# Kernel optimization log

Measured on AMD Instinct MI355X. Metric: run time of the kernel, lower is better.

Reference implementation:

```python
import jax, jax.numpy as jnp
import numpy as np

N_NODES = 20000
N_EDGES = 160000
IN_DIM = 64
HID = 256
EDGE_DIM = 64
SF_DIM = 1  # node_counts_dim = max_cycle - MIN_CYCLE + 1 with MIN_CYCLE==max_cycle (source bug)
N_LAYERS = 3
NUM_GRAPHS = 128
MSG_IN = 2 * HID + 2 * SF_DIM + EDGE_DIM  # 578
UPD_IN = 2 * HID


def setup_inputs() -> dict:
    key = jax.random.key(0)
    ks = jax.random.split(key, 16)
    s = 0.05
    return {
        "x": jax.random.normal(ks[0], (N_NODES, IN_DIM), jnp.float32),
        "node_sf": jax.random.uniform(ks[1], (N_NODES, SF_DIM), jnp.float32),
        "edge_feature": jax.random.normal(ks[2], (N_EDGES, EDGE_DIM), jnp.float32),
        "edge_weight": jax.random.uniform(ks[3], (N_EDGES,), jnp.float32),
        "edge_list": jax.random.randint(ks[4], (N_EDGES, 2), 0, N_NODES, jnp.int32),
        "node2graph": jnp.sort(jax.random.randint(ks[5], (N_NODES,), 0, NUM_GRAPHS, jnp.int32)),
        "Wlin": jax.random.normal(ks[6], (IN_DIM, HID), jnp.float32) * s,
        "blin": jnp.zeros((HID,), jnp.float32),
        "msg_W1": jax.random.normal(ks[7], (N_LAYERS, MSG_IN, HID), jnp.float32) * s,
        "msg_b1": jnp.zeros((N_LAYERS, HID), jnp.float32),
        "msg_W2": jax.random.normal(ks[8], (N_LAYERS, HID, HID), jnp.float32) * s,
        "msg_b2": jnp.zeros((N_LAYERS, HID), jnp.float32),
        "upd_W1": jax.random.normal(ks[9], (N_LAYERS, UPD_IN, HID), jnp.float32) * s,
        "upd_b1": jnp.zeros((N_LAYERS, HID), jnp.float32),
        "upd_W2": jax.random.normal(ks[10], (N_LAYERS, HID, HID), jnp.float32) * s,
        "upd_b2": jnp.zeros((N_LAYERS, HID), jnp.float32),
    }


def reference(x, node_sf, edge_feature, edge_weight, edge_list, node2graph,
              Wlin, blin, msg_W1, msg_b1, msg_W2, msg_b2,
              upd_W1, upd_b1, upd_W2, upd_b2):
    node_in = edge_list[:, 0]
    node_out = edge_list[:, 1]
    h = x @ Wlin + blin  # [N, HID]
    for l in range(N_LAYERS):
        # message: gather endpoint features + structural counts + edge features, 2-layer MLP
        m = jnp.concatenate(
            [h[node_in], h[node_out], node_sf[node_in], node_sf[node_out], edge_feature], axis=-1)
        m = jax.nn.relu(m @ msg_W1[l] + msg_b1[l]) @ msg_W2[l] + msg_b2[l]  # [E, HID]
        # aggregate: weighted scatter-add to destination nodes
        upd = jax.ops.segment_sum(m * edge_weight[:, None], node_out, num_segments=N_NODES)
        # combine: concat + 2-layer MLP, then outer activation
        c = jnp.concatenate([h, upd], axis=-1)
        c = jax.nn.relu(c @ upd_W1[l] + upd_b1[l]) @ upd_W2[l] + upd_b2[l]
        h = jax.nn.relu(c)
    # readout: global add pool per graph
    graph_feature = jax.ops.segment_sum(h, node2graph, num_segments=NUM_GRAPHS)
    return graph_feature
```

## Files before the change

### kernel.cpp

```cpp
#include <hip/hip_runtime.h>
#include <hip/hip_bf16.h>

#define N_NODES   20000
#define N_EDGES   160000
#define IN_DIM    64
#define HID       256
#define EDGE_DIM  64
#define NUM_GRAPHS 128
#define N_LAYERS  3

typedef __attribute__((ext_vector_type(8))) short s16x8;
typedef __attribute__((ext_vector_type(4))) float f32x4;

static __device__ __forceinline__ unsigned short f2bu(float f) {
    union { __hip_bfloat16 h; unsigned short u; } cv;
    cv.h = __float2bfloat16(f);
    return cv.u;
}
static __device__ __forceinline__ s16x8 pack8(const float4 a, const float4 b) {
    s16x8 p;
    p[0] = (short)f2bu(a.x); p[1] = (short)f2bu(a.y);
    p[2] = (short)f2bu(a.z); p[3] = (short)f2bu(a.w);
    p[4] = (short)f2bu(b.x); p[5] = (short)f2bu(b.y);
    p[6] = (short)f2bu(b.z); p[7] = (short)f2bu(b.w);
    return p;
}

#define TILE_SH 8192

__global__ __launch_bounds__(256) void k_deg(const int* __restrict__ el,
                                             int* __restrict__ deg) {
    const int e = blockIdx.x * 256 + threadIdx.x;
    if (e < N_EDGES) atomicAdd(&deg[el[2 * e + 1]], 1);
}

__global__ __launch_bounds__(256) void k_scan(const int* __restrict__ deg,
                                              int* __restrict__ off,
                                              int* __restrict__ cursor) {
    __shared__ int ts[256];
    const int t = threadIdx.x;
    const int base = t * 79;
    const int end  = (base + 79 < N_NODES) ? base + 79 : N_NODES;
    int s = 0;
    for (int i = base; i < end; ++i) s += deg[i];
    ts[t] = s;
    __syncthreads();
    for (int d = 1; d < 256; d <<= 1) {
        const int u = (t >= d) ? ts[t - d] : 0;
        __syncthreads();
        ts[t] += u;
        __syncthreads();
    }
    int run = (t == 0) ? 0 : ts[t - 1];
    for (int i = base; i < end; ++i) {
        off[i] = run; cursor[i] = run; run += deg[i];
    }
}

__global__ __launch_bounds__(256) void k_scat(const int* __restrict__ el,
                                              int* __restrict__ cursor,
                                              int* __restrict__ eidx) {
    const int e = blockIdx.x * 256 + threadIdx.x;
    if (e < N_EDGES) {
        const int d = el[2 * e + 1];
        const int p = atomicAdd(&cursor[d], 1);
        eidx[p] = e;
    }
}

__global__ __launch_bounds__(256) void k_prep(const float* __restrict__ mW1,
                                              const float* __restrict__ mW2,
                                              const float* __restrict__ uW1,
                                              const float* __restrict__ uW2,
                                              unsigned short* __restrict__ msgW1T,
                                              unsigned short* __restrict__ msgW2T,
                                              unsigned short* __restrict__ updW1T,
                                              unsigned short* __restrict__ updW2T) {
    const int b = blockIdx.x;
    const int l = b / 50, t = b % 50;
    const float* W; unsigned short* dst; int rowbase;
    if (t < 18) {
        W = mW1 + (size_t)l * 578 * 256;
        dst = msgW1T + ((size_t)l * 18 + t) * TILE_SH;
        rowbase = (t < 16) ? t * 32 : 514 + (t - 16) * 32;
    } else if (t < 26) {
        const int tt = t - 18;
        W = mW2 + (size_t)l * 65536;
        dst = msgW2T + ((size_t)l * 8 + tt) * TILE_SH;
        rowbase = tt * 32;
    } else if (t < 42) {
        const int tt = t - 26;
        W = uW1 + (size_t)l * 131072;
        dst = updW1T + ((size_t)l * 16 + tt) * TILE_SH;
        rowbase = tt * 32;
    } else {
        const int tt = t - 42;
        W = uW2 + (size_t)l * 65536;
        dst = updW2T + ((size_t)l * 8 + tt) * TILE_SH;
        rowbase = tt * 32;
    }
    const int c = threadIdx.x;
    unsigned short buf[32];
    #pragma unroll
    for (int kk = 0; kk < 32; ++kk)
        buf[kk] = f2bu(W[(size_t)(rowbase + kk) * 256 + c]);
    #pragma unroll
    for (int j = 0; j < 4; ++j)
        *(s16x8*)&dst[(size_t)c * 32 + j * 8] = *(const s16x8*)&buf[j * 8];
}

__global__ __launch_bounds__(256) void k_lin(const float* __restrict__ x,
                                             const float* __restrict__ W,
                                             const float* __restrict__ b,
                                             float* __restrict__ h) {
    __shared__ float Xs[16][68];
    const int tid = threadIdx.x;
    const int n0  = blockIdx.x * 16;
    {
        const int row = tid >> 4, q = tid & 15;
        const float4 v = *(const float4*)&x[(size_t)(n0 + row) * IN_DIM + q * 4];
        Xs[row][q * 4 + 0] = v.x; Xs[row][q * 4 + 1] = v.y;
        Xs[row][q * 4 + 2] = v.z; Xs[row][q * 4 + 3] = v.w;
    }
    __syncthreads();
    const int col = tid;
    float acc[16];
    #pragma unroll
    for (int r = 0; r < 16; ++r) acc[r] = 0.f;
    for (int k = 0; k < IN_DIM; ++k) {
        const float w = W[(size_t)k * HID + col];
        #pragma unroll
        for (int r = 0; r < 16; ++r) acc[r] += Xs[r][k] * w;
    }
    const float bb = b[col];
    #pragma unroll
    for (int r = 0; r < 16; ++r) h[(size_t)(n0 + r) * HID + col] = acc[r] + bb;
}

__global__ __launch_bounds__(256, 3) void k_msg(const float* __restrict__ h,
                                                const float* __restrict__ sf,
                                                const float* __restrict__ ef,
                                                const float* __restrict__ ew,
                                                const int*   __restrict__ el,
                                                const int*   __restrict__ eidx,
                                                const unsigned short* __restrict__ W1T,
                                                const float* __restrict__ W1f,
                                                const float* __restrict__ b1,
                                                const unsigned short* __restrict__ W2T,
                                                const float* __restrict__ b2,
                                                float* __restrict__ upd) {
    __shared__ unsigned short As[2][64 * 40];
    __shared__ __align__(16) unsigned short Ts[64 * 264];
    __shared__ int   Se[64], Sni[64], Sno[64];
    __shared__ float Sew[64], Ssa[64], Ssb[64];

    const int tid = threadIdx.x;
    const int e0  = blockIdx.x * 64;
    if (tid < 64) {
        const int e = eidx[e0 + tid];
        const int a = el[2 * e], bn = el[2 * e + 1];
        Se[tid] = e; Sni[tid] = a; Sno[tid] = bn;
        Sew[tid] = ew[e]; Ssa[tid] = sf[a]; Ssb[tid] = sf[bn];
    }
    __syncthreads();

    const int lane = tid & 63, wv = tid >> 6;
    const int lr = lane & 15, lq = lane >> 4;
    const int arow = tid & 63, aq = tid >> 6;
    const int ni = Sni[arow], no = Sno[arow], myE = Se[arow];

    const unsigned short* bp1 = W1T + ((size_t)(wv * 64 + lr)) * 32 + lq * 8;
    const unsigned short* bp2 = W2T + ((size_t)(wv * 64 + lr)) * 32 + lq * 8;

    f32x4 acc[4][4];
    #pragma unroll
    for (int i = 0; i < 4; ++i)
        #pragma unroll
        for (int j = 0; j < 4; ++j) acc[i][j] = (f32x4)(0.0f);

    {
        const float* asrc = h + (size_t)ni * HID + aq * 8;
        const float4 a0 = *(const float4*)(asrc);
        const float4 a1 = *(const float4*)(asrc + 4);
        *(s16x8*)&As[0][arow * 40 + aq * 8] = pack8(a0, a1);
    }
    s16x8 bfr[4], nbr[4];
    #pragma unroll
    for (int nf = 0; nf < 4; ++nf)
        bfr[nf] = *(const s16x8*)(bp1 + nf * 512);
    __syncthreads();

    for (int s = 0; s < 18; ++s) {
        s16x8 af[4];
        #pragma unroll
        for (int mf = 0; mf < 4; ++mf)
            af[mf] = *(const s16x8*)&As[s & 1][(mf * 16 + lr) * 40 + lq * 8];
        const bool hasNext = (s + 1 < 18);
        float4 nA0, nA1;
        if (hasNext) {
            const int sn = s + 1;
            const float* asrc;
            if (sn < 8)       asrc = h  + (size_t)ni * HID + sn * 32;
            else if (sn < 16) asrc = h  + (size_t)no * HID + (sn - 8) * 32;
            else              asrc = ef + (size_t)myE * EDGE_DIM + (sn - 16) * 32;
            nA0 = *(const float4*)(asrc + aq * 8);
            nA1 = *(const float4*)(asrc + aq * 8 + 4);
            #pragma unroll
            for (int nf = 0; nf < 4; ++nf)
                nbr[nf] = *(const s16x8*)(bp1 + (size_t)sn * TILE_SH + nf * 512);
        }
        #pragma unroll
        for (int mf = 0; mf < 4; ++mf)
            #pragma unroll
            for (int nf = 0; nf < 4; ++nf)
                acc[mf][nf] = __builtin_amdgcn_mfma_f32_16x16x32_bf16(
                    af[mf], bfr[nf], acc[mf][nf], 0, 0, 0);
        if (hasNext) {
            *(s16x8*)&As[(s + 1) & 1][arow * 40 + aq * 8] = pack8(nA0, nA1);
            #pragma unroll
            for (int nf = 0; nf < 4; ++nf) bfr[nf] = nbr[nf];
            __syncthreads();
        }
    }

    #pragma unroll
    for (int nf = 0; nf < 4; ++nf) {
        const int col = wv * 64 + nf * 16 + lr;
        const float w512 = W1f[(size_t)512 * HID + col];
        const float w513 = W1f[(size_t)513 * HID + col];
        const float bb   = b1[col];
        #pragma unroll
        for (int mf = 0; mf < 4; ++mf)
            #pragma unroll
            for (int r = 0; r < 4; ++r) {
                const int row = mf * 16 + lq * 4 + r;
                float v = acc[mf][nf][r] + Ssa[row] * w512 + Ssb[row] * w513 + bb;
                Ts[row * 264 + col] = f2bu(fmaxf(v, 0.f));
            }
    }
    __syncthreads();

    f32x4 acc2[4][4];
    #pragma unroll
    for (int i = 0; i < 4; ++i)
        #pragma unroll
        for (int j = 0; j < 4; ++j) acc2[i][j] = (f32x4)(0.0f);

    s16x8 b2f[4], n2b[4];
    #pragma unroll
    for (int nf = 0; nf < 4; ++nf)
        b2f[nf] = *(const s16x8*)(bp2 + nf * 512);

    for (int s = 0; s < 8; ++s) {
        s16x8 af[4];
        #pragma unroll
        for (int mf = 0; mf < 4; ++mf)
            af[mf] = *(const s16x8*)&Ts[(mf * 16 + lr) * 264 + s * 32 + lq * 8];
        if (s + 1 < 8) {
            #pragma unroll
            for (int nf = 0; nf < 4; ++nf)
                n2b[nf] = *(const s16x8*)(bp2 + (size_t)(s + 1) * TILE_SH + nf * 512);
        }
        #pragma unroll
        for (int mf = 0; mf < 4; ++mf)
            #pragma unroll
            for (int nf = 0; nf < 4; ++nf)
                acc2[mf][nf] = __builtin_amdgcn_mfma_f32_16x16x32_bf16(
                    af[mf], b2f[nf], acc2[mf][nf], 0, 0, 0);
        if (s + 1 < 8) {
            #pragma unroll
            for (int nf = 0; nf < 4; ++nf) b2f[nf] = n2b[nf];
        }
    }

    float* Mf = (float*)Ts;
    #pragma unroll
    for (int half = 0; half < 2; ++half) {
        __syncthreads();
        if ((wv >> 1) == half) {
            #pragma unroll
            for (int nf = 0; nf < 4; ++nf) {
                const int c  = (wv & 1) * 64 + nf * 16 + lr;
                const float bb = b2[half * 128 + c];
                #pragma unroll
                for (int mf = 0; mf < 4; ++mf)
                    #pragma unroll
                    for (int r = 0; r < 4; ++r) {
                        const int row = mf * 16 + lq * 4 + r;
                        Mf[row * 132 + c] = (acc2[mf][nf][r] + bb) * Sew[row];
                    }
            }
        }
        __syncthreads();
        {
            const int c = tid & 127;
            const int colg = half * 128 + c;
            const int rbase = (tid >> 7) * 32;
            float a = 0.f;
            int cur = Sno[rbase];
            for (int r = rbase; r < rbase + 32; ++r) {
                const int g = Sno[r];
                if (g != cur) {
                    atomicAdd(&upd[(size_t)cur * HID + colg], a);
                    a = 0.f; cur = g;
                }
                a += Mf[r * 132 + c];
            }
            atomicAdd(&upd[(size_t)cur * HID + colg], a);
        }
    }
}

__global__ __launch_bounds__(256, 3) void k_upd(const float* __restrict__ h,
                                                const float* __restrict__ upd,
                                                const unsigned short* __restrict__ W1T,
                                                const float* __restrict__ b1,
                                                const unsigned short* __restrict__ W2T,
                                                const float* __restrict__ b2,
                                                float* __restrict__ hout) {
    __shared__ unsigned short As[2][64 * 40];
    __shared__ __align__(16) unsigned short Ts[64 * 264];

    const int tid = threadIdx.x;
    const int n0  = blockIdx.x * 64;
    const int lane = tid & 63, wv = tid >> 6;
    const int lr = lane & 15, lq = lane >> 4;
    const int arow = tid & 63, aq = tid >> 6;
    const int node = (n0 + arow < N_NODES) ? (n0 + arow) : (N_NODES - 1);

    const unsigned short* bp1 = W1T + ((size_t)(wv * 64 + lr)) * 32 + lq * 8;
    const unsigned short* bp2 = W2T + ((size_t)(wv * 64 + lr)) * 32 + lq * 8;

    f32x4 acc[4][4];
    #pragma unroll
    for (int i = 0; i < 4; ++i)
        #pragma unroll
        for (int j = 0; j < 4; ++j) acc[i][j] = (f32x4)(0.0f);

    {
        const float* asrc = h + (size_t)node * HID + aq * 8;
        const float4 a0 = *(const float4*)(asrc);
        const float4 a1 = *(const float4*)(asrc + 4);
        *(s16x8*)&As[0][arow * 40 + aq * 8] = pack8(a0, a1);
    }
    s16x8 bfr[4], nbr[4];
    #pragma unroll
    for (int nf = 0; nf < 4; ++nf)
        bfr[nf] = *(const s16x8*)(bp1 + nf * 512);
    __syncthreads();

    for (int s = 0; s < 16; ++s) {
        s16x8 af[4];
        #pragma unroll
        for (int mf = 0; mf < 4; ++mf)
            af[mf] = *(const s16x8*)&As[s & 1][(mf * 16 + lr) * 40 + lq * 8];
        const bool hasNext = (s + 1 < 16);
        float4 nA0, nA1;
        if (hasNext) {
            const int sn = s + 1;
            const float* asrc = (sn < 8) ? h   + (size_t)node * HID + sn * 32
                                         : upd + (size_t)node * HID + (sn - 8) * 32;
            nA0 = *(const float4*)(asrc + aq * 8);
            nA1 = *(const float4*)(asrc + aq * 8 + 4);
            #pragma unroll
            for (int nf = 0; nf < 4; ++nf)
                nbr[nf] = *(const s16x8*)(bp1 + (size_t)sn * TILE_SH + nf * 512);
        }
        #pragma unroll
        for (int mf = 0; mf < 4; ++mf)
            #pragma unroll
            for (int nf = 0; nf < 4; ++nf)
                acc[mf][nf] = __builtin_amdgcn_mfma_f32_16x16x32_bf16(
                    af[mf], bfr[nf], acc[mf][nf], 0, 0, 0);
        if (hasNext) {
            *(s16x8*)&As[(s + 1) & 1][arow * 40 + aq * 8] = pack8(nA0, nA1);
            #pragma unroll
            for (int nf = 0; nf < 4; ++nf) bfr[nf] = nbr[nf];
            __syncthreads();
        }
    }

    #pragma unroll
    for (int nf = 0; nf < 4; ++nf) {
        const int col = wv * 64 + nf * 16 + lr;
        const float bb = b1[col];
        #pragma unroll
        for (int mf = 0; mf < 4; ++mf)
            #pragma unroll
            for (int r = 0; r < 4; ++r) {
                const int row = mf * 16 + lq * 4 + r;
                Ts[row * 264 + col] = f2bu(fmaxf(acc[mf][nf][r] + bb, 0.f));
            }
    }
    __syncthreads();

    f32x4 acc2[4][4];
    #pragma unroll
    for (int i = 0; i < 4; ++i)
        #pragma unroll
        for (int j = 0; j < 4; ++j) acc2[i][j] = (f32x4)(0.0f);

    s16x8 b2f[4], n2b[4];
    #pragma unroll
    for (int nf = 0; nf < 4; ++nf)
        b2f[nf] = *(const s16x8*)(bp2 + nf * 512);

    for (int s = 0; s < 8; ++s) {
        s16x8 af[4];
        #pragma unroll
        for (int mf = 0; mf < 4; ++mf)
            af[mf] = *(const s16x8*)&Ts[(mf * 16 + lr) * 264 + s * 32 + lq * 8];
        if (s + 1 < 8) {
            #pragma unroll
            for (int nf = 0; nf < 4; ++nf)
                n2b[nf] = *(const s16x8*)(bp2 + (size_t)(s + 1) * TILE_SH + nf * 512);
        }
        #pragma unroll
        for (int mf = 0; mf < 4; ++mf)
            #pragma unroll
            for (int nf = 0; nf < 4; ++nf)
                acc2[mf][nf] = __builtin_amdgcn_mfma_f32_16x16x32_bf16(
                    af[mf], b2f[nf], acc2[mf][nf], 0, 0, 0);
        if (s + 1 < 8) {
            #pragma unroll
            for (int nf = 0; nf < 4; ++nf) b2f[nf] = n2b[nf];
        }
    }

    #pragma unroll
    for (int nf = 0; nf < 4; ++nf) {
        const int col = wv * 64 + nf * 16 + lr;
        const float bb = b2[col];
        #pragma unroll
        for (int mf = 0; mf < 4; ++mf)
            #pragma unroll
            for (int r = 0; r < 4; ++r) {
                const int row = mf * 16 + lq * 4 + r;
                const int n = n0 + row;
                if (n < N_NODES)
                    hout[(size_t)n * HID + col] = fmaxf(acc2[mf][nf][r] + bb, 0.f);
            }
    }
}

__global__ __launch_bounds__(256) void k_graph(const float* __restrict__ h,
                                               const int* __restrict__ n2g,
                                               float* __restrict__ out) {
    __shared__ int Sg[64];
    const int tid = threadIdx.x;
    const int n0  = blockIdx.x * 64;
    if (tid < 64) {
        const int n = n0 + tid;
        Sg[tid] = (n < N_NODES) ? n2g[n] : -1;
    }
    __syncthreads();
    const int col = tid;
    float accv = 0.f;
    int curg = Sg[0];
    for (int r = 0; r < 64; ++r) {
        const int n = n0 + r;
        if (n >= N_NODES) break;
        const int g = Sg[r];
        if (g != curg) {
            atomicAdd(&out[(size_t)curg * HID + col], accv);
            accv = 0.f; curg = g;
        }
        accv += h[(size_t)n * HID + col];
    }
    atomicAdd(&out[(size_t)curg * HID + col], accv);
}

extern "C" void kernel_launch(void* const* d_in, const int* in_sizes, int n_in,
                              void* d_out, int out_size, void* d_ws, size_t ws_size,
                              hipStream_t stream) {
    const float* x    = (const float*)d_in[0];
    const float* sf   = (const float*)d_in[1];
    const float* ef   = (const float*)d_in[2];
    const float* ew   = (const float*)d_in[3];
    const int*   el   = (const int*)d_in[4];
    const int*   n2g  = (const int*)d_in[5];
    const float* Wlin = (const float*)d_in[6];
    const float* blin = (const float*)d_in[7];
    const float* mW1  = (const float*)d_in[8];
    const float* mb1  = (const float*)d_in[9];
    const float* mW2  = (const float*)d_in[10];
    const float* mb2  = (const float*)d_in[11];
    const float* uW1  = (const float*)d_in[12];
    const float* ub1  = (const float*)d_in[13];
    const float* uW2  = (const float*)d_in[14];
    const float* ub2  = (const float*)d_in[15];
    float* out = (float*)d_out;

    float* hA  = (float*)d_ws;
    float* hB  = hA + (size_t)N_NODES * HID;
    float* upd = hB + (size_t)N_NODES * HID;
    unsigned short* wb = (unsigned short*)((char*)d_ws + (size_t)3 * N_NODES * HID * 4);
    unsigned short* msgW1T = wb;
    unsigned short* msgW2T = msgW1T + (size_t)3 * 18 * TILE_SH;
    unsigned short* updW1T = msgW2T + (size_t)3 * 8  * TILE_SH;
    unsigned short* updW2T = updW1T + (size_t)3 * 16 * TILE_SH;
    int* deg    = (int*)(updW2T + (size_t)3 * 8 * TILE_SH);
    int* off    = deg + N_NODES;
    int* cursor = off + N_NODES;
    int* eidx   = cursor + N_NODES;

    hipMemsetAsync(d_out, 0, (size_t)NUM_GRAPHS * HID * sizeof(float), stream);
    hipMemsetAsync(deg, 0, (size_t)N_NODES * sizeof(int), stream);

    k_deg <<<(N_EDGES + 255) / 256, 256, 0, stream>>>(el, deg);
    k_scan<<<1, 256, 0, stream>>>(deg, off, cursor);
    k_scat<<<(N_EDGES + 255) / 256, 256, 0, stream>>>(el, cursor, eidx);

    k_prep<<<150, 256, 0, stream>>>(mW1, mW2, uW1, uW2,
                                    msgW1T, msgW2T, updW1T, updW2T);
    k_lin<<<N_NODES / 16, 256, 0, stream>>>(x, Wlin, blin, hA);

    float* hc = hA;
    float* hn = hB;
    for (int l = 0; l < N_LAYERS; ++l) {
        hipMemsetAsync(upd, 0, (size_t)N_NODES * HID * sizeof(float), stream);
        k_msg<<<N_EDGES / 64, 256, 0, stream>>>(
            hc, sf, ef, ew, el, eidx,
            msgW1T + (size_t)l * 18 * TILE_SH,
            mW1 + (size_t)l * 578 * 256, mb1 + (size_t)l * HID,
            msgW2T + (size_t)l * 8 * TILE_SH, mb2 + (size_t)l * HID, upd);
        k_upd<<<(N_NODES + 63) / 64, 256, 0, stream>>>(
            hc, upd,
            updW1T + (size_t)l * 16 * TILE_SH, ub1 + (size_t)l * HID,
            updW2T + (size_t)l * 8 * TILE_SH,  ub2 + (size_t)l * HID, hn);
        float* t = hc; hc = hn; hn = t;
    }

    k_graph<<<(N_NODES + 63) / 64, 256, 0, stream>>>(hc, n2g, out);
}
```

Before: 597.4 us.

## Store node and edge features in bf16 and load MFMA operands directly from global

Node hidden states and edge features are now kept in bf16: h is written as bf16 by the linear and update kernels, and a new pre-pass converts the edge features once. The message and update kernels drop the shared-memory A staging buffer and its per-step barrier, and instead gather bf16 MFMA A fragments straight from global memory into registers with a register double buffer. This halves gather traffic for the irregular per-edge row gathers and removes the LDS round trip and syncs. The trade-off is extra bf16 rounding of the stored hidden state between layers and less coalesced 16-byte global loads per lane.

New measurement: 721.4 us. 20.8% more time.

```diff
diff --git a/kernel.cpp b/kernel.cpp
--- a/kernel.cpp
+++ b/kernel.cpp
@@ -16,6 +16,11 @@
     union { __hip_bfloat16 h; unsigned short u; } cv;
     cv.h = __float2bfloat16(f);
     return cv.u;
+}
+static __device__ __forceinline__ float bu2f(unsigned short u) {
+    union { float f; unsigned int i; } c;
+    c.i = ((unsigned int)u) << 16;
+    return c.f;
 }
 static __device__ __forceinline__ s16x8 pack8(const float4 a, const float4 b) {
     s16x8 p;
@@ -109,10 +114,18 @@
         *(s16x8*)&dst[(size_t)c * 32 + j * 8] = *(const s16x8*)&buf[j * 8];
 }
 
+__global__ __launch_bounds__(256) void k_pef(const float* __restrict__ ef,
+                                             unsigned short* __restrict__ efbf) {
+    const size_t i = ((size_t)blockIdx.x * 256 + threadIdx.x) * 8;
+    const float4 a = *(const float4*)&ef[i];
+    const float4 b = *(const float4*)&ef[i + 4];
+    *(s16x8*)&efbf[i] = pack8(a, b);
+}
+
 __global__ __launch_bounds__(256) void k_lin(const float* __restrict__ x,
                                              const float* __restrict__ W,
                                              const float* __restrict__ b,
-                                             float* __restrict__ h) {
+                                             unsigned short* __restrict__ h) {
     __shared__ float Xs[16][68];
     const int tid = threadIdx.x;
     const int n0  = blockIdx.x * 16;
@@ -134,12 +147,13 @@
     }
     const float bb = b[col];
     #pragma unroll
-    for (int r = 0; r < 16; ++r) h[(size_t)(n0 + r) * HID + col] = acc[r] + bb;
-}
-
-__global__ __launch_bounds__(256, 3) void k_msg(const float* __restrict__ h,
+    for (int r = 0; r < 16; ++r)
+        h[(size_t)(n0 + r) * HID + col] = f2bu(acc[r] + bb);
+}
+
+__global__ __launch_bounds__(256, 3) void k_msg(const unsigned short* __restrict__ hbf,
                                                 const float* __restrict__ sf,
-                                                const float* __restrict__ ef,
+                                                const unsigned short* __restrict__ efbf,
                                                 const float* __restrict__ ew,
                                                 const int*   __restrict__ el,
                                                 const int*   __restrict__ eidx,
@@ -149,7 +163,6 @@
                                                 const unsigned short* __restrict__ W2T,
                                                 const float* __restrict__ b2,
                                                 float* __restrict__ upd) {
-    __shared__ unsigned short As[2][64 * 40];
     __shared__ __align__(16) unsigned short Ts[64 * 264];
     __shared__ int   Se[64], Sni[64], Sno[64];
     __shared__ float Sew[64], Ssa[64], Ssb[64];
@@ -166,11 +179,16 @@
 
     const int lane = tid & 63, wv = tid >> 6;
     const int lr = lane & 15, lq = lane >> 4;
-    const int arow = tid & 63, aq = tid >> 6;
-    const int ni = Sni[arow], no = Sno[arow], myE = Se[arow];
-
-    const unsigned short* bp1 = W1T + ((size_t)(wv * 64 + lr)) * 32 + lq * 8;
-    const unsigned short* bp2 = W2T + ((size_t)(wv * 64 + lr)) * 32 + lq * 8;
+
+    int rni[4], rno[4], rfe[4];
+    #pragma unroll
+    for (int mf = 0; mf < 4; ++mf) {
+        const int row = mf * 16 + lr;
+        rni[mf] = Sni[row]; rno[mf] = Sno[row]; rfe[mf] = Se[row];
+    }
+
+    const unsigned short* bp1 = W1T + (size_t)(wv * 64 + lr) * 32 + lq * 8;
+    const unsigned short* bp2 = W2T + (size_t)(wv * 64 + lr) * 32 + lq * 8;
 
     f32x4 acc[4][4];
     #pragma unroll
@@ -178,36 +196,28 @@
         #pragma unroll
         for (int j = 0; j < 4; ++j) acc[i][j] = (f32x4)(0.0f);
 
-    {
-        const float* asrc = h + (size_t)ni * HID + aq * 8;
-        const float4 a0 = *(const float4*)(asrc);
-        const float4 a1 = *(const float4*)(asrc + 4);
-        *(s16x8*)&As[0][arow * 40 + aq * 8] = pack8(a0, a1);
-    }
-    s16x8 bfr[4], nbr[4];
+    s16x8 af[4], bfr[4], na[4], nb[4];
+    #pragma unroll
+    for (int mf = 0; mf < 4; ++mf)
+        af[mf] = *(const s16x8*)(hbf + (size_t)rni[mf] * HID + lq * 8);
     #pragma unroll
     for (int nf = 0; nf < 4; ++nf)
         bfr[nf] = *(const s16x8*)(bp1 + nf * 512);
-    __syncthreads();
 
     for (int s = 0; s < 18; ++s) {
-        s16x8 af[4];
-        #pragma unroll
-        for (int mf = 0; mf < 4; ++mf)
-            af[mf] = *(const s16x8*)&As[s & 1][(mf * 16 + lr) * 40 + lq * 8];
-        const bool hasNext = (s + 1 < 18);
-        float4 nA0, nA1;
-        if (hasNext) {
+        if (s + 1 < 18) {
             const int sn = s + 1;
-            const float* asrc;
-            if (sn < 8)       asrc = h  + (size_t)ni * HID + sn * 32;
-            else if (sn < 16) asrc = h  + (size_t)no * HID + (sn - 8) * 32;
-            else              asrc = ef + (size_t)myE * EDGE_DIM + (sn - 16) * 32;
-            nA0 = *(const float4*)(asrc + aq * 8);
-            nA1 = *(const float4*)(asrc + aq * 8 + 4);
-            #pragma unroll
-            for (int nf = 0; nf < 4; ++nf)
-                nbr[nf] = *(const s16x8*)(bp1 + (size_t)sn * TILE_SH + nf * 512);
+            #pragma unroll
+            for (int mf = 0; mf < 4; ++mf) {
+                const unsigned short* ap;
+                if (sn < 8)       ap = hbf  + (size_t)rni[mf] * HID + sn * 32;
+                else if (sn < 16) ap = hbf  + (size_t)rno[mf] * HID + (sn - 8) * 32;
+                else              ap = efbf + (size_t)rfe[mf] * EDGE_DIM + (sn - 16) * 32;
+                na[mf] = *(const s16x8*)(ap + lq * 8);
+            }
+            #pragma unroll
+            for (int nf = 0; nf < 4; ++nf)
+                nb[nf] = *(const s16x8*)(bp1 + (size_t)sn * TILE_SH + nf * 512);
         }
         #pragma unroll
         for (int mf = 0; mf < 4; ++mf)
@@ -215,11 +225,11 @@
             for (int nf = 0; nf < 4; ++nf)
                 acc[mf][nf] = __builtin_amdgcn_mfma_f32_16x16x32_bf16(
                     af[mf], bfr[nf], acc[mf][nf], 0, 0, 0);
-        if (hasNext) {
-            *(s16x8*)&As[(s + 1) & 1][arow * 40 + aq * 8] = pack8(nA0, nA1);
-            #pragma unroll
-            for (int nf = 0; nf < 4; ++nf) bfr[nf] = nbr[nf];
-            __syncthreads();
+        if (s + 1 < 18) {
+            #pragma unroll
+            for (int mf = 0; mf < 4; ++mf) af[mf] = na[mf];
+            #pragma unroll
+            for (int nf = 0; nf < 4; ++nf) bfr[nf] = nb[nf];
         }
     }
 
@@ -252,10 +262,10 @@
         b2f[nf] = *(const s16x8*)(bp2 + nf * 512);
 
     for (int s = 0; s < 8; ++s) {
-        s16x8 af[4];
-        #pragma unroll
-        for (int mf = 0; mf < 4; ++mf)
-            af[mf] = *(const s16x8*)&Ts[(mf * 16 + lr) * 264 + s * 32 + lq * 8];
+        s16x8 a2[4];
+        #pragma unroll
+        for (int mf = 0; mf < 4; ++mf)
+            a2[mf] = *(const s16x8*)&Ts[(mf * 16 + lr) * 264 + s * 32 + lq * 8];
         if (s + 1 < 8) {
             #pragma unroll
             for (int nf = 0; nf < 4; ++nf)
@@ -266,7 +276,7 @@
             #pragma unroll
             for (int nf = 0; nf < 4; ++nf)
                 acc2[mf][nf] = __builtin_amdgcn_mfma_f32_16x16x32_bf16(
-                    af[mf], b2f[nf], acc2[mf][nf], 0, 0, 0);
+                    a2[mf], b2f[nf], acc2[mf][nf], 0, 0, 0);
         if (s + 1 < 8) {
             #pragma unroll
             for (int nf = 0; nf < 4; ++nf) b2f[nf] = n2b[nf];
@@ -311,25 +321,29 @@
     }
 }
 
-__global__ __launch_bounds__(256, 3) void k_upd(const float* __restrict__ h,
+__global__ __launch_bounds__(256, 3) void k_upd(const unsigned short* __restrict__ hbf,
                                                 const float* __restrict__ upd,
                                                 const unsigned short* __restrict__ W1T,
                                                 const float* __restrict__ b1,
                                                 const unsigned short* __restrict__ W2T,
                                                 const float* __restrict__ b2,
-                                                float* __restrict__ hout) {
-    __shared__ unsigned short As[2][64 * 40];
+                                                unsigned short* __restrict__ hout) {
     __shared__ __align__(16) unsigned short Ts[64 * 264];
 
     const int tid = threadIdx.x;
     const int n0  = blockIdx.x * 64;
     const int lane = tid & 63, wv = tid >> 6;
     const int lr = lane & 15, lq = lane >> 4;
-    const int arow = tid & 63, aq = tid >> 6;
-    const int node = (n0 + arow < N_NODES) ? (n0 + arow) : (N_NODES - 1);
-
-    const unsigned short* bp1 = W1T + ((size_t)(wv * 64 + lr)) * 32 + lq * 8;
-    const unsigned short* bp2 = W2T + ((size_t)(wv * 64 + lr)) * 32 + lq * 8;
+
+    int nrow[4];
+    #pragma unroll
+    for (int mf = 0; mf < 4; ++mf) {
+        const int n = n0 + mf * 16 + lr;
+        nrow[mf] = (n < N_NODES) ? n : (N_NODES - 1);
+    }
+
+    const unsigned short* bp1 = W1T + (size_t)(wv * 64 + lr) * 32 + lq * 8;
+    const unsigned short* bp2 = W2T + (size_t)(wv * 64 + lr) * 32 + lq * 8;
 
     f32x4 acc[4][4];
     #pragma unroll
@@ -337,34 +351,31 @@
         #pragma unroll
         for (int j = 0; j < 4; ++j) acc[i][j] = (f32x4)(0.0f);
 
-    {
-        const float* asrc = h + (size_t)node * HID + aq * 8;
-        const float4 a0 = *(const float4*)(asrc);
-        const float4 a1 = *(const float4*)(asrc + 4);
-        *(s16x8*)&As[0][arow * 40 + aq * 8] = pack8(a0, a1);
-    }
-    s16x8 bfr[4], nbr[4];
+    s16x8 af[4], bfr[4], na[4], nb[4];
+    #pragma unroll
+    for (int mf = 0; mf < 4; ++mf)
+        af[mf] = *(const s16x8*)(hbf + (size_t)nrow[mf] * HID + lq * 8);
     #pragma unroll
     for (int nf = 0; nf < 4; ++nf)
         bfr[nf] = *(const s16x8*)(bp1 + nf * 512);
-    __syncthreads();
 
     for (int s = 0; s < 16; ++s) {
-        s16x8 af[4];
-        #pragma unroll
-        for (int mf = 0; mf < 4; ++mf)
-            af[mf] = *(const s16x8*)&As[s & 1][(mf * 16 + lr) * 40 + lq * 8];
-        const bool hasNext = (s + 1 < 16);
-        float4 nA0, nA1;
-        if (hasNext) {
+        if (s + 1 < 16) {
             const int sn = s + 1;
-            const float* asrc = (sn < 8) ? h   + (size_t)node * HID + sn * 32
-                                         : upd + (size_t)node * HID + (sn - 8) * 32;
-            nA0 = *(const float4*)(asrc + aq * 8);
-            nA1 = *(const float4*)(asrc + aq * 8 + 4);
-            #pragma unroll
-            for (int nf = 0; nf < 4; ++nf)
-                nbr[nf] = *(const s16x8*)(bp1 + (size_t)sn * TILE_SH + nf * 512);
+            if (sn < 8) {
+                #pragma unroll
+                for (int mf = 0; mf < 4; ++mf)
+                    na[mf] = *(const s16x8*)(hbf + (size_t)nrow[mf] * HID + sn * 32 + lq * 8);
+            } else {
+                #pragma unroll
+                for (int mf = 0; mf < 4; ++mf) {
+                    const float* up = upd + (size_t)nrow[mf] * HID + (sn - 8) * 32 + lq * 8;
+                    na[mf] = pack8(*(const float4*)up, *(const float4*)(up + 4));
+                }
+            }
+            #pragma unroll
+            for (int nf = 0; nf < 4; ++nf)
+                nb[nf] = *(const s16x8*)(bp1 + (size_t)sn * TILE_SH + nf * 512);
         }
         #pragma unroll
         for (int mf = 0; mf < 4; ++mf)
@@ -372,11 +383,11 @@
             for (int nf = 0; nf < 4; ++nf)
                 acc[mf][nf] = __builtin_amdgcn_mfma_f32_16x16x32_bf16(
                     af[mf], bfr[nf], acc[mf][nf], 0, 0, 0);
-        if (hasNext) {
-            *(s16x8*)&As[(s + 1) & 1][arow * 40 + aq * 8] = pack8(nA0, nA1);
-            #pragma unroll
-            for (int nf = 0; nf < 4; ++nf) bfr[nf] = nbr[nf];
-            __syncthreads();
+        if (s + 1 < 16) {
+            #pragma unroll
+            for (int mf = 0; mf < 4; ++mf) af[mf] = na[mf];
+            #pragma unroll
+            for (int nf = 0; nf < 4; ++nf) bfr[nf] = nb[nf];
         }
     }
 
@@ -406,10 +417,10 @@
         b2f[nf] = *(const s16x8*)(bp2 + nf * 512);
 
     for (int s = 0; s < 8; ++s) {
-        s16x8 af[4];
-        #pragma unroll
-        for (int mf = 0; mf < 4; ++mf)
-            af[mf] = *(const s16x8*)&Ts[(mf * 16 + lr) * 264 + s * 32 + lq * 8];
+        s16x8 a2[4];
+        #pragma unroll
+        for (int mf = 0; mf < 4; ++mf)
+            a2[mf] = *(const s16x8*)&Ts[(mf * 16 + lr) * 264 + s * 32 + lq * 8];
         if (s + 1 < 8) {
             #pragma unroll
             for (int nf = 0; nf < 4; ++nf)
@@ -420,7 +431,7 @@
             #pragma unroll
             for (int nf = 0; nf < 4; ++nf)
                 acc2[mf][nf] = __builtin_amdgcn_mfma_f32_16x16x32_bf16(
-                    af[mf], b2f[nf], acc2[mf][nf], 0, 0, 0);
+                    a2[mf], b2f[nf], acc2[mf][nf], 0, 0, 0);
         if (s + 1 < 8) {
             #pragma unroll
             for (int nf = 0; nf < 4; ++nf) b2f[nf] = n2b[nf];
@@ -438,12 +449,12 @@
                 const int row = mf * 16 + lq * 4 + r;
                 const int n = n0 + row;
                 if (n < N_NODES)
-                    hout[(size_t)n * HID + col] = fmaxf(acc2[mf][nf][r] + bb, 0.f);
-            }
-    }
-}
-
-__global__ __launch_bounds__(256) void k_graph(const float* __restrict__ h,
+                    hout[(size_t)n * HID + col] = f2bu(fmaxf(acc2[mf][nf][r] + bb, 0.f));
+            }
+    }
+}
+
+__global__ __launch_bounds__(256) void k_graph(const unsigned short* __restrict__ h,
                                                const int* __restrict__ n2g,
                                                float* __restrict__ out) {
     __shared__ int Sg[64];
@@ -465,7 +476,7 @@
             atomicAdd(&out[(size_t)curg * HID + col], accv);
             accv = 0.f; curg = g;
         }
-        accv += h[(size_t)n * HID + col];
+        accv += bu2f(h[(size_t)n * HID + col]);
     }
     atomicAdd(&out[(size_t)curg * HID + col], accv);
 }
@@ -491,15 +502,15 @@
     const float* ub2  = (const float*)d_in[15];
     float* out = (float*)d_out;
 
-    float* hA  = (float*)d_ws;
-    float* hB  = hA + (size_t)N_NODES * HID;
-    float* upd = hB + (size_t)N_NODES * HID;
-    unsigned short* wb = (unsigned short*)((char*)d_ws + (size_t)3 * N_NODES * HID * 4);
-    unsigned short* msgW1T = wb;
+    unsigned short* hA   = (unsigned short*)d_ws;
+    unsigned short* hB   = hA + (size_t)N_NODES * HID;
+    unsigned short* efbf = hB + (size_t)N_NODES * HID;
+    unsigned short* msgW1T = efbf + (size_t)N_EDGES * EDGE_DIM;
     unsigned short* msgW2T = msgW1T + (size_t)3 * 18 * TILE_SH;
     unsigned short* updW1T = msgW2T + (size_t)3 * 8  * TILE_SH;
     unsigned short* updW2T = updW1T + (size_t)3 * 16 * TILE_SH;
-    int* deg    = (int*)(updW2T + (size_t)3 * 8 * TILE_SH);
+    float* upd  = (float*)(updW2T + (size_t)3 * 8 * TILE_SH);
+    int* deg    = (int*)(upd + (size_t)N_NODES * HID);
     int* off    = deg + N_NODES;
     int* cursor = off + N_NODES;
     int* eidx   = cursor + N_NODES;
@@ -513,14 +524,15 @@
 
     k_prep<<<150, 256, 0, stream>>>(mW1, mW2, uW1, uW2,
                                     msgW1T, msgW2T, updW1T, updW2T);
-    k_lin<<<N_NODES / 16, 256, 0, stream>>>(x, Wlin, blin, hA);
-
-    float* hc = hA;
-    float* hn = hB;
+    k_pef <<<N_EDGES * EDGE_DIM / (256 * 8), 256, 0, stream>>>(ef, efbf);
+    k_lin <<<N_NODES / 16, 256, 0, stream>>>(x, Wlin, blin, hA);
+
+    unsigned short* hc = hA;
+    unsigned short* hn = hB;
     for (int l = 0; l < N_LAYERS; ++l) {
         hipMemsetAsync(upd, 0, (size_t)N_NODES * HID * sizeof(float), stream);
         k_msg<<<N_EDGES / 64, 256, 0, stream>>>(
-            hc, sf, ef, ew, el, eidx,
+            hc, sf, efbf, ew, el, eidx,
             msgW1T + (size_t)l * 18 * TILE_SH,
             mW1 + (size_t)l * 578 * 256, mb1 + (size_t)l * HID,
             msgW2T + (size_t)l * 8 * TILE_SH, mb2 + (size_t)l * HID, upd);
@@ -528,7 +540,7 @@
             hc, upd,
             updW1T + (size_t)l * 16 * TILE_SH, ub1 + (size_t)l * HID,
             updW2T + (size_t)l * 8 * TILE_SH,  ub2 + (size_t)l * HID, hn);
-        float* t = hc; hc = hn; hn = t;
+        unsigned short* t = hc; hc = hn; hn = t;
     }
 
     k_graph<<<(N_NODES + 63) / 64, 256, 0, stream>>>(hc, n2g, out);
```
